# Optimization experiments

Measured on AMD Instinct MI355X. Metric: run time of the kernel, lower is better.

The kernel has to match this reference:

```python
import jax, jax.numpy as jnp
import numpy as np

B, L, D = 32768, 50, 50      # batch, components per sample, feat_dim
R, C = 3, 10                 # r-combination size, out_cnt combos per sample
VOCAB, OUT = 100000, 1       # comp_cnt, output_size


def setup_inputs() -> dict:
    key = jax.random.key(0)
    k1, k2, k3, k4, k5 = jax.random.split(key, 5)
    x = jax.random.randint(k1, (B, L), 0, VOCAB, dtype=jnp.int64)
    emb_mask = jax.random.uniform(k2, (B, L, 1), dtype=jnp.float32)
    combo_idx = jax.random.randint(k3, (B, C, R), 0, L, dtype=jnp.int64)
    emb_table = jax.random.normal(k4, (VOCAB, D), dtype=jnp.float32)
    W = jax.random.normal(k5, (OUT, R * D), dtype=jnp.float32) * 0.02
    b = jnp.zeros((OUT,), dtype=jnp.float32)
    return {"x": x, "emb_mask": emb_mask, "combo_idx": combo_idx,
            "step": 0, "emb_table": emb_table, "W": W, "b": b}


def reference(x, emb_mask, combo_idx, step, emb_table, W, b):
    # Embedding lookup + mask: [B, L, D]
    emb = emb_table[x] * emb_mask
    Bb, Ll, Dd = emb.shape
    Cc, Rr = combo_idx.shape[1], combo_idx.shape[2]
    # Gather the R rows for each of the C combos: [B, C*R, D] -> [B, C, R*D]
    flat_idx = combo_idx.reshape(Bb, Cc * Rr)[..., None]
    vecs = jnp.take_along_axis(emb, flat_idx, axis=1).reshape(Bb, Cc, Rr * Dd)
    # Tiny linear + sigmoid per combo, then sum over combos: [B, OUT]
    act = jax.nn.sigmoid(jnp.einsum('bcf,of->bco', vecs, W) + b)
    return act.sum(axis=1)
```

## Files before the change

### kernel.cpp

```cpp
#include <hip/hip_runtime.h>
#include <math.h>

#define LL 50
#define DD 50
#define RR 3
#define CC 10

__global__ __launch_bounds__(256) void precompute_dots_kernel(
    const float* __restrict__ emb_table,
    const float* __restrict__ W,
    float4*      __restrict__ dtab,
    int vocab)
{
    __shared__ float sW[RR * DD];
    if (threadIdx.x < RR * DD) sW[threadIdx.x] = W[threadIdx.x];
    __syncthreads();

    const int tid = blockIdx.x * 256 + threadIdx.x;
    const int r   = tid >> 2;
    const int q   = tid & 3;
    if (r >= vocab) return;

    const float2* p = reinterpret_cast<const float2*>(emb_table + (size_t)r * DD);
    const int s = 6 * q + (q > 0 ? 1 : 0);
    const int c = (q == 0) ? 7 : 6;

    float d0 = 0.f, d1 = 0.f, d2 = 0.f;
    #pragma unroll
    for (int k = 0; k < 7; ++k) {
        if (k < c) {
            float2 e = p[s + k];
            int j = 2 * (s + k);
            d0 = fmaf(e.x, sW[          j], fmaf(e.y, sW[          j + 1], d0));
            d1 = fmaf(e.x, sW[    DD  + j], fmaf(e.y, sW[    DD  + j + 1], d1));
            d2 = fmaf(e.x, sW[2 * DD  + j], fmaf(e.y, sW[2 * DD  + j + 1], d2));
        }
    }
    d0 += __shfl_xor(d0, 1); d0 += __shfl_xor(d0, 2);
    d1 += __shfl_xor(d1, 1); d1 += __shfl_xor(d1, 2);
    d2 += __shfl_xor(d2, 1); d2 += __shfl_xor(d2, 2);
    if (q == 0) dtab[r] = make_float4(d0, d1, d2, 0.f);
}

__global__ __launch_bounds__(256) void fused_combo_kernel(
    const int*    __restrict__ x,
    const float*  __restrict__ emb_mask,
    const int*    __restrict__ combo_idx,
    const float4* __restrict__ dtab,
    const float*  __restrict__ bvec,
    float*        __restrict__ out,
    int B)
{
    const int tid  = threadIdx.x;
    const int w    = tid >> 6;
    const int lane = tid & 63;
    const int b    = blockIdx.x * 4 + w;
    if (b >= B) return;

    int ci = 0;
    if (lane < CC * RR) ci = combo_idx[b * (CC * RR) + lane];

    unsigned long long um = (lane < CC * RR) ? (1ull << ci) : 0ull;
    um |= __shfl_xor(um, 32);
    um |= __shfl_xor(um, 16);
    um |= __shfl_xor(um,  8);
    um |= __shfl_xor(um,  4);
    um |= __shfl_xor(um,  2);
    um |= __shfl_xor(um,  1);
    const bool used = (lane < LL) && ((um >> lane) & 1ull);

    float d0 = 0.f, d1 = 0.f, d2 = 0.f;
    if (lane < LL) {
        int   row = x[b * LL + lane];
        float m   = emb_mask[b * LL + lane];
        if (used) {
            float4 d = dtab[row];
            d0 = d.x * m; d1 = d.y * m; d2 = d.z * m;
        }
    }

    int i0 = __shfl(ci, 3 * lane    ) & 63;
    int i1 = __shfl(ci, 3 * lane + 1) & 63;
    int i2 = __shfl(ci, 3 * lane + 2) & 63;

    float sacc = __shfl(d0, i0) + __shfl(d1, i1) + __shfl(d2, i2) + bvec[0];
    float v = (lane < CC) ? 1.0f / (1.0f + __expf(-sacc)) : 0.f;

    v += __shfl_down(v, 8);
    v += __shfl_down(v, 4);
    v += __shfl_down(v, 2);
    v += __shfl_down(v, 1);
    if (lane == 0) out[b] = v;
}

extern "C" void kernel_launch(void* const* d_in, const int* in_sizes, int n_in,
                              void* d_out, int out_size, void* d_ws, size_t ws_size,
                              hipStream_t stream) {
    const int*   x         = (const int*)d_in[0];
    const float* emb_mask  = (const float*)d_in[1];
    const int*   combo_idx = (const int*)d_in[2];
    const float* emb_table = (const float*)d_in[4];
    const float* W         = (const float*)d_in[5];
    const float* bvec      = (const float*)d_in[6];
    float*       out       = (float*)d_out;

    const int B     = out_size;
    const int vocab = in_sizes[4] / DD;

    float4* dtab = (float4*)d_ws;

    const int pc_threads = 4 * vocab;
    precompute_dots_kernel<<<(pc_threads + 255) / 256, 256, 0, stream>>>(
        emb_table, W, dtab, vocab);

    fused_combo_kernel<<<(B + 3) / 4, 256, 0, stream>>>(
        x, emb_mask, combo_idx, dtab, bvec, out, B);
}
```

Measured before the change: 23.23 us.

## Evaluate combos per lane with 4 samples per wavefront, direct scalar gathers

Restructures the combo kernel so each wavefront handles four samples, with one lane per combo. Each lane gathers its three component indices, token ids and mask values itself and reads single floats from the dot table, replacing the per-lane load of all fifty components and the cross-lane shuffles. This cuts the number of wavefronts and skips dot-table reads for unused rows. In exchange it makes scattered, uncoalesced per-lane gathers with possible repeated reads, and 6 of every 16 lanes sit idle.

Measured after the change: 19.20 us. 17.4% less time.

```diff
diff --git a/kernel.cpp b/kernel.cpp
--- a/kernel.cpp
+++ b/kernel.cpp
@@ -42,55 +42,42 @@
     if (q == 0) dtab[r] = make_float4(d0, d1, d2, 0.f);
 }
 
-__global__ __launch_bounds__(256) void fused_combo_kernel(
+__global__ __launch_bounds__(256) void combo_eval_kernel(
     const int*    __restrict__ x,
     const float*  __restrict__ emb_mask,
     const int*    __restrict__ combo_idx,
-    const float4* __restrict__ dtab,
+    const float*  __restrict__ dtabf,
     const float*  __restrict__ bvec,
     float*        __restrict__ out,
     int B)
 {
-    const int tid  = threadIdx.x;
-    const int w    = tid >> 6;
-    const int lane = tid & 63;
-    const int b    = blockIdx.x * 4 + w;
-    if (b >= B) return;
+    const int lane = threadIdx.x & 63;
+    const int gw   = blockIdx.x * 4 + (threadIdx.x >> 6);
+    const int s    = lane >> 4;
+    const int c    = lane & 15;
+    const int b    = gw * 4 + s;
 
-    int ci = 0;
-    if (lane < CC * RR) ci = combo_idx[b * (CC * RR) + lane];
-
-    unsigned long long um = (lane < CC * RR) ? (1ull << ci) : 0ull;
-    um |= __shfl_xor(um, 32);
-    um |= __shfl_xor(um, 16);
-    um |= __shfl_xor(um,  8);
-    um |= __shfl_xor(um,  4);
-    um |= __shfl_xor(um,  2);
-    um |= __shfl_xor(um,  1);
-    const bool used = (lane < LL) && ((um >> lane) & 1ull);
-
-    float d0 = 0.f, d1 = 0.f, d2 = 0.f;
-    if (lane < LL) {
-        int   row = x[b * LL + lane];
-        float m   = emb_mask[b * LL + lane];
-        if (used) {
-            float4 d = dtab[row];
-            d0 = d.x * m; d1 = d.y * m; d2 = d.z * m;
-        }
+    float v = 0.f;
+    if (b < B && c < CC) {
+        const size_t cb = ((size_t)b * CC + c) * RR;
+        int i0 = combo_idx[cb + 0];
+        int i1 = combo_idx[cb + 1];
+        int i2 = combo_idx[cb + 2];
+        const int*   xr = x        + b * LL;
+        const float* mr = emb_mask + b * LL;
+        int   r0 = xr[i0], r1 = xr[i1], r2 = xr[i2];
+        float m0 = mr[i0], m1 = mr[i1], m2 = mr[i2];
+        float sacc = dtabf[4 * r0 + 0] * m0
+                   + dtabf[4 * r1 + 1] * m1
+                   + dtabf[4 * r2 + 2] * m2
+                   + bvec[0];
+        v = 1.0f / (1.0f + __expf(-sacc));
     }
-
-    int i0 = __shfl(ci, 3 * lane    ) & 63;
-    int i1 = __shfl(ci, 3 * lane + 1) & 63;
-    int i2 = __shfl(ci, 3 * lane + 2) & 63;
-
-    float sacc = __shfl(d0, i0) + __shfl(d1, i1) + __shfl(d2, i2) + bvec[0];
-    float v = (lane < CC) ? 1.0f / (1.0f + __expf(-sacc)) : 0.f;
-
     v += __shfl_down(v, 8);
     v += __shfl_down(v, 4);
     v += __shfl_down(v, 2);
     v += __shfl_down(v, 1);
-    if (lane == 0) out[b] = v;
+    if (c == 0 && b < B) out[b] = v;
 }
 
 extern "C" void kernel_launch(void* const* d_in, const int* in_sizes, int n_in,
@@ -113,6 +100,7 @@
     precompute_dots_kernel<<<(pc_threads + 255) / 256, 256, 0, stream>>>(
         emb_table, W, dtab, vocab);
 
-    fused_combo_kernel<<<(B + 3) / 4, 256, 0, stream>>>(
-        x, emb_mask, combo_idx, dtab, bvec, out, B);
+    const int samples_per_block = 16;
+    combo_eval_kernel<<<(B + samples_per_block - 1) / samples_per_block, 256, 0, stream>>>(
+        x, emb_mask, combo_idx, (const float*)dtab, bvec, out, B);
 }
```
